# Kernel tuning notes

Measured on AMD Instinct MI355X. Metric: run time of the kernel, lower is better.

The kernel has to match this reference:

```python
import jax, jax.numpy as jnp
import numpy as np

SEQ, BATCH, HID, OUT = 2048, 128, 256, 2

def setup_inputs() -> dict:
    key = jax.random.key(0)
    ks = jax.random.split(key, 8)
    x = jax.random.normal(ks[0], (SEQ, BATCH), dtype=jnp.float32)
    h0 = jax.random.normal(ks[1], (BATCH, HID), dtype=jnp.float32) * 0.1
    noise = jax.random.normal(ks[2], (SEQ, BATCH, HID), dtype=jnp.float32) * 0.1
    W_ih = jax.random.normal(ks[3], (HID, 1), dtype=jnp.float32) * 0.1 + 0.5
    W_hh = jax.random.normal(ks[4], (HID, HID), dtype=jnp.float32) * 0.4
    W_hh_bias = jax.random.normal(ks[5], (HID, HID), dtype=jnp.float32) * 0.1 + 0.1
    b_h = jnp.zeros((HID,), dtype=jnp.float32)
    W = jax.random.normal(ks[6], (OUT, HID), dtype=jnp.float32) * 0.3
    b = jnp.zeros((OUT,), dtype=jnp.float32)
    return dict(x=x, h0=h0, noise=noise, W_ih=W_ih, W_hh=W_hh,
                W_hh_bias=W_hh_bias, b_h=b_h, W=W, b=b, context=1)

def reference(x, h0, noise, W_ih, W_hh, W_hh_bias, b_h, W, b, context):
    # input_size == 1, so x_t @ W_ih.T is an outer product with W_ih[:, 0]
    w_in = W_ih[:, 0]                       # (hid,)
    # context is a scalar, so c1 transposes cancel: W_eff = W_hh + context*W_hh_bias
    W_eff = W_hh + context * W_hh_bias      # (hid, hid)

    def step(h, inp):
        x_t, n_t = inp                      # (batch,), (batch, hid)
        h = jnp.tanh(h @ W_eff.T + x_t[:, None] * w_in[None, :] + b_h) + n_t
        return h, h

    _, out = jax.lax.scan(step, h0, (x, noise))   # (seq, batch, hid)
    out = jnp.transpose(out, (1, 0, 2))           # (batch, seq, hid)
    y = jax.nn.sigmoid(jnp.einsum('bsh,oh->bso', out, W) + b)
    return y[:, :, 0], out
```

## Files before the change

kernel.cpp:

```cpp
#include <hip/hip_runtime.h>
#include <math.h>

#define SEQ   2048
#define BATCH 128
#define HID   256


__global__ __launch_bounds__(512, 2) void rnn_kernel(
    const float* __restrict__ x,
    const float* __restrict__ h0,
    const float* __restrict__ noise,
    const float* __restrict__ W_ih,
    const float* __restrict__ W_hh,
    const float* __restrict__ W_hhb,
    const float* __restrict__ b_h,
    const float* __restrict__ Wy,
    const float* __restrict__ by,
    const int*   __restrict__ ctx,
    float* __restrict__ h_out,
    float* __restrict__ y_out)
{
    const int b    = blockIdx.x;
    const int tid  = threadIdx.x;
    const int w    = tid >> 6;
    const int lane = tid & 63;
    const int jg   = lane >> 3;
    const int kg   = lane & 7;
    const int j0   = w * 32 + jg * 4;
    const int jres = j0 + (kg & 3);

    __shared__ __align__(16) float hbuf[2][HID];
    __shared__ float ywave[2][8];

    int iv = *ctx;
    float c = (iv > 1000000 || iv < -1000000) ? __int_as_float(iv) : (float)iv;

    float wreg[4][32];
    #pragma unroll
    for (int e = 0; e < 4; ++e) {
        const float4* wr  = (const float4*)&W_hh [(j0 + e) * HID + kg * 32];
        const float4* wrb = (const float4*)&W_hhb[(j0 + e) * HID + kg * 32];
        #pragma unroll
        for (int q = 0; q < 8; ++q) {
            float4 av = wr[q], bv = wrb[q];
            wreg[e][4*q+0] = av.x + c * bv.x;
            wreg[e][4*q+1] = av.y + c * bv.y;
            wreg[e][4*q+2] = av.z + c * bv.z;
            wreg[e][4*q+3] = av.w + c * bv.w;
        }
    }

    const float win = W_ih[jres];
    const float bh  = b_h[jres];
    const float w0  = Wy[jres];
    const float b0v = by[0];

    if (tid < HID) {
        int cc = tid >> 5, ii = (tid >> 2) & 7, ee = tid & 3;
        hbuf[0][cc * 32 + (((ii + cc) & 7) << 2) + ee] = h0[b * HID + tid];
    }

    int voff[8];
    #pragma unroll
    for (int i = 0; i < 8; ++i)
        voff[i] = kg * 128 + (((i + kg) & 7) << 4);

    const int  b0k = kg & 1;
    const int  b1k = (kg >> 1) & 1;
    const bool wr4 = (kg < 4);
    const int  wslot = w * 32 + (((jg + w) & 7) << 2) + kg;

    float x_next = x[b];
    float n_next = noise[(size_t)b * HID + jres];
    const float* xp = x + BATCH + b;
    const float* np = noise + ((size_t)BATCH + b) * HID + jres;

    float* hop = h_out + (size_t)b * SEQ * HID;
    float* yp  = y_out + (size_t)b * SEQ;

    __syncthreads();

#define STEP(T, CUR)                                                         \
  {                                                                          \
    const float x_t = x_next;                                                \
    const float n_t = n_next;                                                \
    x_next = *xp;                                                            \
    n_next = *np;                                                            \
    if ((T) + 2 < SEQ) { xp += BATCH; np += (size_t)BATCH * HID; }           \
    const char* hb = (const char*)&hbuf[CUR][0];                             \
    float p0 = 0.f, p1 = 0.f, p2 = 0.f, p3 = 0.f;                            \
    _Pragma("unroll")                                                        \
    for (int i = 0; i < 8; ++i) {                                            \
      float4 h4 = *(const float4*)(hb + voff[i]);                            \
      p0 = fmaf(h4.x, wreg[0][4*i+0], p0);                                   \
      p0 = fmaf(h4.y, wreg[0][4*i+1], p0);                                   \
      p0 = fmaf(h4.z, wreg[0][4*i+2], p0);                                   \
      p0 = fmaf(h4.w, wreg[0][4*i+3], p0);                                   \
      p1 = fmaf(h4.x, wreg[1][4*i+0], p1);                                   \
      p1 = fmaf(h4.y, wreg[1][4*i+1], p1);                                   \
      p1 = fmaf(h4.z, wreg[1][4*i+2], p1);                                   \
      p1 = fmaf(h4.w, wreg[1][4*i+3], p1);                                   \
      p2 = fmaf(h4.x, wreg[2][4*i+0], p2);                                   \
      p2 = fmaf(h4.y, wreg[2][4*i+1], p2);                                   \
      p2 = fmaf(h4.z, wreg[2][4*i+2], p2);                                   \
      p2 = fmaf(h4.w, wreg[2][4*i+3], p2);                                   \
      p3 = fmaf(h4.x, wreg[3][4*i+0], p3);                                   \
      p3 = fmaf(h4.y, wreg[3][4*i+1], p3);                                   \
      p3 = fmaf(h4.z, wreg[3][4*i+2], p3);                                   \
      p3 = fmaf(h4.w, wreg[3][4*i+3], p3);                                   \
    }                                                                        \
     \
    if (w == ((T) & 7) && (T) > 0) {                                         \
      float s = (lane < 8) ? ywave[(CUR) ^ 1][lane] : 0.f;                   \
      s += __shfl_xor(s, 1, 64);                                             \
      s += __shfl_xor(s, 2, 64);                                             \
      s += __shfl_xor(s, 4, 64);                                             \
      if (lane == 0) yp[(T) - 1] = 1.f / (1.f + __expf(-(s + b0v)));         \
    }                                                                        \
     \
    float m0 = b0k ? p1 : p0,  s0 = b0k ? p0 : p1;                           \
    float m1 = b0k ? p3 : p2,  s1 = b0k ? p2 : p3;                           \
    float q0 = m0 + __shfl_xor(s0, 1, 64);                                   \
    float q1 = m1 + __shfl_xor(s1, 1, 64);                                   \
    float mm = b1k ? q1 : q0,  ss = b1k ? q0 : q1;                           \
    float r  = mm + __shfl_xor(ss, 2, 64);                                   \
    r += __shfl_xor(r, 4, 64);                                               \
    float z  = fmaf(x_t, win, r) + bh;                                       \
    float ex = __expf(2.f * z);              \
    float hn = 1.f - 2.f / (ex + 1.f) + n_t;                                 \
    if (wr4) {                                                               \
      hbuf[(CUR) ^ 1][wslot] = hn;       \
      hop[jres] = hn;                                                        \
    }                                                                        \
                               \
    float qy = wr4 ? hn * w0 : 0.f;                                          \
    qy += __shfl_xor(qy, 1, 64);                                             \
    qy += __shfl_xor(qy, 2, 64);                                             \
    qy += __shfl_xor(qy, 4, 64);                                             \
    qy += __shfl_xor(qy, 8, 64);                                             \
    qy += __shfl_xor(qy, 16, 64);                                            \
    qy += __shfl_xor(qy, 32, 64);                                            \
    if (lane == 0) ywave[CUR][w] = qy;                                       \
    hop += HID;                                                              \
    __syncthreads();                                                         \
  }

    for (int t = 0; t < SEQ; t += 2) {
        STEP(t, 0)
        STEP(t + 1, 1)
    }

    if (w == 0) {
        float s = (lane < 8) ? ywave[1][lane] : 0.f;
        s += __shfl_xor(s, 1, 64);
        s += __shfl_xor(s, 2, 64);
        s += __shfl_xor(s, 4, 64);
        if (lane == 0) yp[SEQ - 1] = 1.f / (1.f + __expf(-(s + b0v)));
    }
#undef STEP
}

extern "C" void kernel_launch(void* const* d_in, const int* in_sizes, int n_in,
                              void* d_out, int out_size, void* d_ws, size_t ws_size,
                              hipStream_t stream) {
    const float* x     = (const float*)d_in[0];
    const float* h0    = (const float*)d_in[1];
    const float* noise = (const float*)d_in[2];
    const float* W_ih  = (const float*)d_in[3];
    const float* W_hh  = (const float*)d_in[4];
    const float* W_hhb = (const float*)d_in[5];
    const float* b_h   = (const float*)d_in[6];
    const float* W     = (const float*)d_in[7];
    const float* bvec  = (const float*)d_in[8];
    const int*   ctx   = (const int*)d_in[9];

    float* y_out = (float*)d_out;
    float* h_out = (float*)d_out + (size_t)BATCH * SEQ;

    rnn_kernel<<<dim3(BATCH), dim3(512), 0, stream>>>(
        x, h0, noise, W_ih, W_hh, W_hhb, b_h, W, bvec, ctx, h_out, y_out);
}
```

Baseline: 2.596 ms.

## Replace cross-lane shuffles with DPP ops, lighten barrier, deepen noise prefetch

```diff
diff --git a/kernel.cpp b/kernel.cpp
--- a/kernel.cpp
+++ b/kernel.cpp
@@ -5,6 +5,18 @@
 #define BATCH 128
 #define HID   256
 
+#define DPP_XOR1  0xB1
+#define DPP_XOR2  0x4E
+#define DPP_XOR7  0x141
+#define DPP_XOR15 0x140
+template<int CTRL>
+__device__ __forceinline__ float dppf(float v) {
+    return __builtin_bit_cast(float, __builtin_amdgcn_update_dpp(
+        0, __builtin_bit_cast(int, v), CTRL, 0xF, 0xF, true));
+}
+
+#define BARRIER() do { asm volatile("s_waitcnt lgkmcnt(0)" ::: "memory"); \
+                       __builtin_amdgcn_s_barrier(); } while (0)
 
 __global__ __launch_bounds__(512, 2) void rnn_kernel(
     const float* __restrict__ x,
@@ -30,7 +42,7 @@
     const int jres = j0 + (kg & 3);
 
     __shared__ __align__(16) float hbuf[2][HID];
-    __shared__ float ywave[2][8];
+    __shared__ __align__(16) float ywave[2][32];
 
     int iv = *ctx;
     float c = (iv > 1000000 || iv < -1000000) ? __int_as_float(iv) : (float)iv;
@@ -70,10 +82,12 @@
     const bool wr4 = (kg < 4);
     const int  wslot = w * 32 + (((jg + w) & 7) << 2) + kg;
 
-    float x_next = x[b];
-    float n_next = noise[(size_t)b * HID + jres];
-    const float* xp = x + BATCH + b;
-    const float* np = noise + ((size_t)BATCH + b) * HID + jres;
+    float x_next  = x[b];
+    float n_next  = noise[(size_t)b * HID + jres];
+    float x_next2 = x[BATCH + b];
+    float n_next2 = noise[((size_t)BATCH + b) * HID + jres];
+    const float* xp = x + 2 * BATCH + b;
+    const float* np = noise + ((size_t)2 * BATCH + b) * HID + jres;
 
     float* hop = h_out + (size_t)b * SEQ * HID;
     float* yp  = y_out + (size_t)b * SEQ;
@@ -84,9 +98,9 @@
   {                                                                          \
     const float x_t = x_next;                                                \
     const float n_t = n_next;                                                \
-    x_next = *xp;                                                            \
-    n_next = *np;                                                            \
-    if ((T) + 2 < SEQ) { xp += BATCH; np += (size_t)BATCH * HID; }           \
+    x_next = x_next2;  n_next = n_next2;                                     \
+    x_next2 = *xp;     n_next2 = *np;                                        \
+    if ((T) + 3 < SEQ) { xp += BATCH; np += (size_t)BATCH * HID; }           \
     const char* hb = (const char*)&hbuf[CUR][0];                             \
     float p0 = 0.f, p1 = 0.f, p2 = 0.f, p3 = 0.f;                            \
     _Pragma("unroll")                                                        \
@@ -111,20 +125,25 @@
     }                                                                        \
      \
     if (w == ((T) & 7) && (T) > 0) {                                         \
-      float s = (lane < 8) ? ywave[(CUR) ^ 1][lane] : 0.f;                   \
-      s += __shfl_xor(s, 1, 64);                                             \
-      s += __shfl_xor(s, 2, 64);                                             \
-      s += __shfl_xor(s, 4, 64);                                             \
+      float4 yv = *(const float4*)&ywave[(CUR) ^ 1][(lane & 7) * 4];         \
+      float s = (yv.x + yv.y) + (yv.z + yv.w);                               \
+      s += dppf<DPP_XOR1>(s);                                                \
+      s += dppf<DPP_XOR2>(s);                                                \
+      s += dppf<DPP_XOR7>(s);                                                \
       if (lane == 0) yp[(T) - 1] = 1.f / (1.f + __expf(-(s + b0v)));         \
     }                                                                        \
-     \
+    \
+    \
+    p0 += dppf<DPP_XOR7>(p0);                                                \
+    p1 += dppf<DPP_XOR7>(p1);                                                \
+    p2 += dppf<DPP_XOR7>(p2);                                                \
+    p3 += dppf<DPP_XOR7>(p3);                                                \
     float m0 = b0k ? p1 : p0,  s0 = b0k ? p0 : p1;                           \
     float m1 = b0k ? p3 : p2,  s1 = b0k ? p2 : p3;                           \
-    float q0 = m0 + __shfl_xor(s0, 1, 64);                                   \
-    float q1 = m1 + __shfl_xor(s1, 1, 64);                                   \
+    float q0 = m0 + dppf<DPP_XOR1>(s0);                                      \
+    float q1 = m1 + dppf<DPP_XOR1>(s1);                                      \
     float mm = b1k ? q1 : q0,  ss = b1k ? q0 : q1;                           \
-    float r  = mm + __shfl_xor(ss, 2, 64);                                   \
-    r += __shfl_xor(r, 4, 64);                                               \
+    float r  = mm + dppf<DPP_XOR2>(ss);                                      \
     float z  = fmaf(x_t, win, r) + bh;                                       \
     float ex = __expf(2.f * z);              \
     float hn = 1.f - 2.f / (ex + 1.f) + n_t;                                 \
@@ -132,17 +151,15 @@
       hbuf[(CUR) ^ 1][wslot] = hn;       \
       hop[jres] = hn;                                                        \
     }                                                                        \
-                               \
+    \
     float qy = wr4 ? hn * w0 : 0.f;                                          \
-    qy += __shfl_xor(qy, 1, 64);                                             \
-    qy += __shfl_xor(qy, 2, 64);                                             \
-    qy += __shfl_xor(qy, 4, 64);                                             \
-    qy += __shfl_xor(qy, 8, 64);                                             \
-    qy += __shfl_xor(qy, 16, 64);                                            \
-    qy += __shfl_xor(qy, 32, 64);                                            \
-    if (lane == 0) ywave[CUR][w] = qy;                                       \
+    qy += dppf<DPP_XOR1>(qy);                                                \
+    qy += dppf<DPP_XOR2>(qy);                                                \
+    qy += dppf<DPP_XOR7>(qy);                                                \
+    qy += dppf<DPP_XOR15>(qy);                                               \
+    if ((lane & 15) == 0) ywave[CUR][w * 4 + (lane >> 4)] = qy;              \
     hop += HID;                                                              \
-    __syncthreads();                                                         \
+    BARRIER();                                                               \
   }
 
     for (int t = 0; t < SEQ; t += 2) {
@@ -151,10 +168,11 @@
     }
 
     if (w == 0) {
-        float s = (lane < 8) ? ywave[1][lane] : 0.f;
-        s += __shfl_xor(s, 1, 64);
-        s += __shfl_xor(s, 2, 64);
-        s += __shfl_xor(s, 4, 64);
+        float4 yv = *(const float4*)&ywave[1][(lane & 7) * 4];
+        float s = (yv.x + yv.y) + (yv.z + yv.w);
+        s += dppf<DPP_XOR1>(s);
+        s += dppf<DPP_XOR2>(s);
+        s += dppf<DPP_XOR7>(s);
         if (lane == 0) yp[SEQ - 1] = 1.f / (1.f + __expf(-(s + b0v)));
     }
 #undef STEP
```

Result: faster. 2.231 ms (-14.1%).
